# Optimization experiments

Measured on AMD Instinct MI355X. Metric: run time of the kernel, lower is better.

## Reference

```python
import jax, jax.numpy as jnp
import numpy as np

EPS_NORM = 1e-8   # torch cosine_similarity norm eps
EPS_DEN = 1e-10
CLAMP_MAX = 1e10


def _cos_matrix(a, b):
    # rows of a vs rows of b: [Na, Nb] cosine similarity via normalized matmul
    an = a / jnp.clip(jnp.linalg.norm(a, axis=-1, keepdims=True), EPS_NORM)
    bn = b / jnp.clip(jnp.linalg.norm(b, axis=-1, keepdims=True), EPS_NORM)
    return an @ bn.T


def setup_inputs() -> dict:
    key = jax.random.key(0)
    k1, k2, k3, k4, k5 = jax.random.split(key, 5)
    N, D, M, C = 4096, 256, 2, 100
    return {
        "label_encodings": jax.random.normal(k1, (N, D), dtype=jnp.float32),
        "fusion_z": jax.random.normal(k2, (M, N, D), dtype=jnp.float32),
        "sample_embeddings": jax.random.normal(k3, (N, D), dtype=jnp.float32),
        "label_embeddings": jax.random.normal(k4, (N, D), dtype=jnp.float32),
        "labels": jax.random.randint(k5, (N,), 0, C, dtype=jnp.int64),
        "temperature": jnp.ones((), dtype=jnp.float32),
        "xi": jnp.ones((), dtype=jnp.float32),
    }


def reference(label_encodings, fusion_z, sample_embeddings, label_embeddings,
              labels, temperature, xi):
    # ---- class_prompt_contrastive_Learning ----
    sim = _cos_matrix(label_encodings, label_encodings)            # [N, N]
    e = jnp.minimum(jnp.exp(sim / temperature), CLAMP_MAX)
    mask = (labels[:, None] == labels[None, :])
    num = jnp.sum(e * mask, axis=1)
    den = jnp.clip(jnp.sum(e, axis=1), EPS_DEN)
    loss_class = jnp.mean(-jnp.log(num / den))

    # ---- supervised_cross_view_contrastive ----
    M, N, D = fusion_z.shape
    fz = fusion_z.reshape(M * N, D)
    lab_exp = jnp.tile(labels, M)                                  # labels.repeat(M)
    mask2 = (lab_exp[:, None] == lab_exp[None, :])
    sim2 = _cos_matrix(fz, fz)                                     # [MN, MN]
    e2 = jnp.exp(sim2 / temperature)
    num2 = jnp.sum(e2 * mask2, axis=1)
    den2 = jnp.clip(jnp.sum(e2, axis=1), EPS_DEN)
    loss_cross = jnp.mean(-jnp.log(num2 / den2))

    # ---- boundary_aware_independent_hashing ----
    cs = _cos_matrix(sample_embeddings, label_embeddings)          # [N, N]
    Dm = (1.0 - cs) * 0.5
    y = (labels[:, None] == labels[None, :]).astype(cs.dtype)
    loss_mat = y * Dm ** 2 + (1.0 - y) * jnp.maximum(xi - Dm, 0.0) ** 2
    loss_hash = jnp.mean(loss_mat)

    return jnp.stack([loss_class, loss_cross, loss_hash])
```

## Files before the change

### kernel.cpp

```cpp
#include <hip/hip_runtime.h>
#include <hip/hip_bf16.h>
#include <stdint.h>


typedef __attribute__((ext_vector_type(8))) short bf16x8;
typedef __attribute__((ext_vector_type(4))) float f32x4;

__device__ inline void gload_lds16(const void* g, void* l) {
  __builtin_amdgcn_global_load_lds(
      (__attribute__((address_space(1))) void*)g,
      (__attribute__((address_space(3))) void*)l, 16, 0, 0);
}

__device__ inline void barrier_raw() {
  asm volatile("" ::: "memory");
  __builtin_amdgcn_s_barrier();
  asm volatile("" ::: "memory");
}

__device__ inline unsigned short f2bf(float x) {
  unsigned int u = __builtin_bit_cast(unsigned int, x);
  u = (u + 0x7fffu + ((u >> 16) & 1u)) >> 16;
  return (unsigned short)u;
}

__global__ __launch_bounds__(256) void norm_kernel(
    const float* __restrict__ LE, const float* __restrict__ FZ,
    const float* __restrict__ SE, const float* __restrict__ LM,
    unsigned short* __restrict__ An, unsigned short* __restrict__ Fn,
    unsigned short* __restrict__ Sn, unsigned short* __restrict__ Ln,
    float* __restrict__ hacc, float* __restrict__ out) {
  const int tid = threadIdx.x;
  if (blockIdx.x == 0) {
    if (tid == 0) out[0] = 0.f;
    if (tid == 1) out[1] = 0.f;
    if (tid == 2) hacc[0] = 0.f;
  }

  const int wid = tid >> 6, lane = tid & 63;
  const int row = blockIdx.x * 4 + wid;

  const float* src;
  unsigned short* dst;
  int r;
  if (row < 4096)       { src = LE; dst = An; r = row; }
  else if (row < 12288) { src = FZ; dst = Fn; r = row - 4096; }
  else if (row < 16384) { src = SE; dst = Sn; r = row - 12288; }
  else                  { src = LM; dst = Ln; r = row - 16384; }

  const float4 v = *(const float4*)(src + (size_t)r * 256 + lane * 4);
  float ss = v.x * v.x + v.y * v.y + v.z * v.z + v.w * v.w;
#pragma unroll
  for (int m = 1; m < 64; m <<= 1) ss += __shfl_xor(ss, m);
  const float scale = 1.0f / fmaxf(sqrtf(ss), 1e-8f);

  ushort4 o;
  o.x = f2bf(v.x * scale);
  o.y = f2bf(v.y * scale);
  o.z = f2bf(v.z * scale);
  o.w = f2bf(v.w * scale);
  *(ushort4*)(dst + (size_t)r * 256 + lane * 4) = o;
}

__device__ inline void tri_decode(int t, int nb, int& rb, int& cb) {
  int r = 0;
  while (t >= nb - r) { t -= nb - r; ++r; }
  rb = r;
  cb = r + t;
}

__global__ __launch_bounds__(256, 2) void fused_sim(
    const unsigned short* __restrict__ An, const unsigned short* __restrict__ Fn,
    const unsigned short* __restrict__ Sn, const unsigned short* __restrict__ Ln,
    const int* __restrict__ labels,
    const float* __restrict__ tp, const float* __restrict__ xip,
    float2* __restrict__ Pc,
    float2* __restrict__ Px,
    float* __restrict__ hacc) {
  __shared__ __align__(16) char Ab[2][16384];
  __shared__ __align__(16) char Bb[2][16384];
  __shared__ int lrS[128], lcS[128];

  const int hw = blockIdx.x;
  const int bid = (hw & 7) * 454 + (hw >> 3);

  int mode, rb, cb;
  const unsigned short *X, *Y;
  if (bid < 528) {
    mode = 0; tri_decode(bid, 32, rb, cb); X = An; Y = An;
  } else if (bid < 2608) {
    mode = 1; tri_decode(bid - 528, 64, rb, cb); X = Fn; Y = Fn;
  } else {
    mode = 2; const int t = bid - 2608; rb = t >> 5; cb = t & 31;
    X = Sn; Y = Ln;
  }

  const int tid = threadIdx.x;
  const int lane = tid & 63, wid = tid >> 6;
  const int wr = wid >> 1, wc = wid & 1;
  const int g = lane >> 4, c = lane & 15;

  int mylab = labels[(tid < 128 ? rb * 128 + tid : cb * 128 + tid - 128) & 4095];

  f32x4 acc[4][4];
  const f32x4 zero = {0.f, 0.f, 0.f, 0.f};
#pragma unroll
  for (int m = 0; m < 4; ++m)
#pragma unroll
    for (int n = 0; n < 4; ++n) acc[m][n] = zero;

  const int srow = tid >> 3;
  const int sgl = (tid & 7) ^ (srow & 7);
  const char* xs = (const char*)X + ((size_t)rb * 128 + srow) * 512 + sgl * 16;
  const char* ys = (const char*)Y + ((size_t)cb * 128 + srow) * 512 + sgl * 16;

#define STAGE(KK, BUF)                                                    \
  do {                                                                    \
    const char* xa = xs + (KK) * 128;                                     \
    const char* ya = ys + (KK) * 128;                                     \
    char* da = (char*)(&Ab[(BUF)][0]) + wid * 1024;                       \
    char* db = (char*)(&Bb[(BUF)][0]) + wid * 1024;                       \
    gload_lds16(xa, da);                                                  \
    gload_lds16(xa + 16384, da + 4096);                                   \
    gload_lds16(xa + 32768, da + 8192);                                   \
    gload_lds16(xa + 49152, da + 12288);                                  \
    gload_lds16(ya, db);                                                  \
    gload_lds16(ya + 16384, db + 4096);                                   \
    gload_lds16(ya + 32768, db + 8192);                                   \
    gload_lds16(ya + 49152, db + 12288);                                  \
  } while (0)

  STAGE(0, 0);
  STAGE(1, 1);
  asm volatile("" : "+v"(mylab));

  const int pxs = c & 7;
  const int aoff = (wr * 64 + c) * 128;
  const int boff = (wc * 64 + c) * 128;

#pragma unroll
  for (int kk = 0; kk < 4; ++kk) {
    if (kk < 3) asm volatile("s_waitcnt vmcnt(8)" ::: "memory");
    else        asm volatile("s_waitcnt vmcnt(0)" ::: "memory");
    barrier_raw();
    if (kk == 0) {
      if (tid < 128) lrS[tid] = mylab;
      else           lcS[tid - 128] = mylab;
    }
    const char* ab = (const char*)(&Ab[kk & 1][0]) + aoff;
    const char* bb = (const char*)(&Bb[kk & 1][0]) + boff;
#pragma unroll
    for (int ks = 0; ks < 2; ++ks) {
      const int px = ((ks * 4 + g) ^ pxs) * 16;
      bf16x8 af[4], bg[4];
#pragma unroll
      for (int m = 0; m < 4; ++m) af[m] = *(const bf16x8*)(ab + m * 2048 + px);
#pragma unroll
      for (int n = 0; n < 4; ++n) bg[n] = *(const bf16x8*)(bb + n * 2048 + px);
      __builtin_amdgcn_s_setprio(1);
#pragma unroll
      for (int m = 0; m < 4; ++m)
#pragma unroll
        for (int n = 0; n < 4; ++n)
          acc[m][n] = __builtin_amdgcn_mfma_f32_16x16x32_bf16(
              af[m], bg[n], acc[m][n], 0, 0, 0);
      __builtin_amdgcn_s_setprio(0);
    }
    barrier_raw();
    if (kk < 2) STAGE(kk + 2, kk & 1);
  }
#undef STAGE

  float* sc = (float*)(&Ab[0][0]);
  if (mode < 2) {
    const float invt = 1.0f / tp[0];
    const bool docol = (rb != cb);
    float2* Pp = (mode == 0) ? Pc : Px;
    const int NR = (mode == 0) ? 4096 : 8192;
    int collab[4];
#pragma unroll
    for (int n = 0; n < 4; ++n) collab[n] = lcS[wc * 64 + n * 16 + c];

    float* rowN = sc, *rowD = sc + 256, *colN = sc + 512, *colD = sc + 768;
    float cn[4] = {0.f, 0.f, 0.f, 0.f}, cd[4] = {0.f, 0.f, 0.f, 0.f};
    float rn[16], rd[16];
#pragma unroll
    for (int m = 0; m < 4; ++m) {
#pragma unroll
      for (int reg = 0; reg < 4; ++reg) {
        const int rlab = lrS[wr * 64 + m * 16 + g * 4 + reg];
        float pn = 0.f, pd = 0.f;
#pragma unroll
        for (int n = 0; n < 4; ++n) {
          float e = __expf(acc[m][n][reg] * invt);
          if (mode == 0) e = fminf(e, 1e10f);
          pd += e;
          const float en = (rlab == collab[n]) ? e : 0.f;
          pn += en;
          cd[n] += e;
          cn[n] += en;
        }
#pragma unroll
        for (int msk = 1; msk < 16; msk <<= 1) {
          pn += __shfl_xor(pn, msk);
          pd += __shfl_xor(pd, msk);
        }
        rn[m * 4 + reg] = pn;
        rd[m * 4 + reg] = pd;
      }
    }
    if (c == 0) {
#pragma unroll
      for (int m = 0; m < 4; ++m)
#pragma unroll
        for (int reg = 0; reg < 4; ++reg) {
          const int rloc = wr * 64 + m * 16 + g * 4 + reg;
          rowN[wc * 128 + rloc] = rn[m * 4 + reg];
          rowD[wc * 128 + rloc] = rd[m * 4 + reg];
        }
    }
#pragma unroll
    for (int n = 0; n < 4; ++n) {
      float a = cn[n], b = cd[n];
      a += __shfl_xor(a, 16); b += __shfl_xor(b, 16);
      a += __shfl_xor(a, 32); b += __shfl_xor(b, 32);
      if (g == 0) {
        colN[wr * 128 + wc * 64 + n * 16 + c] = a;
        colD[wr * 128 + wc * 64 + n * 16 + c] = b;
      }
    }
    __syncthreads();
    if (tid < 128) {
      Pp[(size_t)cb * NR + rb * 128 + tid] =
          make_float2(rowN[tid] + rowN[128 + tid], rowD[tid] + rowD[128 + tid]);
    } else if (docol) {
      const int t2 = tid - 128;
      Pp[(size_t)rb * NR + cb * 128 + t2] =
          make_float2(colN[t2] + colN[128 + t2], colD[t2] + colD[128 + t2]);
    }
  } else {
    const float xi = xip[0];
    int collab[4];
#pragma unroll
    for (int n = 0; n < 4; ++n) collab[n] = lcS[wc * 64 + n * 16 + c];
    float part = 0.f;
#pragma unroll
    for (int m = 0; m < 4; ++m)
#pragma unroll
      for (int reg = 0; reg < 4; ++reg) {
        const int rlab = lrS[wr * 64 + m * 16 + g * 4 + reg];
#pragma unroll
        for (int n = 0; n < 4; ++n) {
          const float cs = acc[m][n][reg];
          const float Dm = (1.0f - cs) * 0.5f;
          const float u = fmaxf(xi - Dm, 0.0f);
          part += (rlab == collab[n]) ? Dm * Dm : u * u;
        }
      }
#pragma unroll
    for (int msk = 1; msk < 64; msk <<= 1) part += __shfl_xor(part, msk);
    if (lane == 0) sc[wid] = part;
    __syncthreads();
    if (tid == 0) atomicAdd(hacc, sc[0] + sc[1] + sc[2] + sc[3]);
  }
}

__global__ __launch_bounds__(256) void finalize_kernel(
    const float2* __restrict__ Pc, const float2* __restrict__ Px,
    const float* __restrict__ hacc, float* __restrict__ out) {
  const int b = blockIdx.x, tid = threadIdx.x;
  const float2* P;
  int nslots, NR, row, oi;
  if (b < 16) { P = Pc; nslots = 32; NR = 4096; row = b * 256 + tid; oi = 0; }
  else { P = Px; nslots = 64; NR = 8192; row = (b - 16) * 256 + tid; oi = 1; }
  float n = 0.f, d = 0.f;
  for (int s = 0; s < nslots; ++s) {
    const float2 v = P[(size_t)s * NR + row];
    n += v.x;
    d += v.y;
  }
  float val = -logf(n / fmaxf(d, 1e-10f));
#pragma unroll
  for (int m = 1; m < 64; m <<= 1) val += __shfl_xor(val, m);
  __shared__ float r[4];
  if ((tid & 63) == 0) r[tid >> 6] = val;
  __syncthreads();
  if (tid == 0) atomicAdd(&out[oi], (r[0] + r[1] + r[2] + r[3]) / (float)NR);
  if (b == 0 && tid == 0) out[2] = hacc[0] * (1.0f / 16777216.0f);
}

extern "C" void kernel_launch(void* const* d_in, const int* in_sizes, int n_in,
                              void* d_out, int out_size, void* d_ws,
                              size_t ws_size, hipStream_t stream) {
  const float* LE = (const float*)d_in[0];
  const float* FZ = (const float*)d_in[1];
  const float* SE = (const float*)d_in[2];
  const float* LM = (const float*)d_in[3];
  const int* labels = (const int*)d_in[4];
  const float* tp = (const float*)d_in[5];
  const float* xip = (const float*)d_in[6];
  float* out = (float*)d_out;

  char* ws = (char*)d_ws;
  unsigned short* An = (unsigned short*)(ws);
  unsigned short* Fn = (unsigned short*)(ws + 2097152);
  unsigned short* Sn = (unsigned short*)(ws + 6291456);
  unsigned short* Ln = (unsigned short*)(ws + 8388608);
  float2* Pc = (float2*)(ws + 10485760);
  float2* Px = (float2*)(ws + 11534336);
  float* hacc = (float*)(ws + 15728640);

  norm_kernel<<<dim3(5120), dim3(256), 0, stream>>>(LE, FZ, SE, LM, An, Fn,
                                                    Sn, Ln, hacc, out);
  fused_sim<<<dim3(3632), dim3(256), 0, stream>>>(An, Fn, Sn, Ln, labels, tp,
                                                  xip, Pc, Px, hacc);
  finalize_kernel<<<dim3(48), dim3(256), 0, stream>>>(Pc, Px, hacc, out);
}
```

Baseline: 166.9 us.

## Enlarge similarity tiles to 256x256 with 512-thread blocks and interleaved prefetch

Moves the fused similarity kernel from 128x128 tiles with 256 threads to 256x256 tiles with 512 threads (8 waves, each computing a 128x64 sub-tile). The next K-slice is now prefetched inside the MFMA phases instead of after a trailing barrier, and labels are loaded straight into LDS. The aim is to halve global/L2 traffic per output, cut the number of blocks and triangular partial slots (which also shrinks the finalize reduction), and reduce barrier count. In exchange it uses 128KB+ of LDS per block, so only one block fits per CU, and it needs more accumulator registers. The 920-block grid gives less wave-level load balancing across CUs.

```diff
diff --git a/kernel.cpp b/kernel.cpp
--- a/kernel.cpp
+++ b/kernel.cpp
@@ -10,12 +10,6 @@
   __builtin_amdgcn_global_load_lds(
       (__attribute__((address_space(1))) void*)g,
       (__attribute__((address_space(3))) void*)l, 16, 0, 0);
-}
-
-__device__ inline void barrier_raw() {
-  asm volatile("" ::: "memory");
-  __builtin_amdgcn_s_barrier();
-  asm volatile("" ::: "memory");
 }
 
 __device__ inline unsigned short f2bf(float x) {
@@ -69,7 +63,7 @@
   cb = r + t;
 }
 
-__global__ __launch_bounds__(256, 2) void fused_sim(
+__global__ __launch_bounds__(512) void fused_sim(
     const unsigned short* __restrict__ An, const unsigned short* __restrict__ Fn,
     const unsigned short* __restrict__ Sn, const unsigned short* __restrict__ Ln,
     const int* __restrict__ labels,
@@ -77,103 +71,119 @@
     float2* __restrict__ Pc,
     float2* __restrict__ Px,
     float* __restrict__ hacc) {
-  __shared__ __align__(16) char Ab[2][16384];
-  __shared__ __align__(16) char Bb[2][16384];
-  __shared__ int lrS[128], lcS[128];
+  __shared__ __align__(16) char AB[131072];
+  __shared__ __align__(16) int labS[512];
+  __shared__ float sN[1024], sD[1024];
+  __shared__ float cN[512], cD[512];
+
+  const int tid = threadIdx.x;
+  const int lane = tid & 63, wid = tid >> 6;
+  const int wr = wid >> 2, wc = wid & 3;
+  const int g = lane >> 4, c = lane & 15;
 
   const int hw = blockIdx.x;
-  const int bid = (hw & 7) * 454 + (hw >> 3);
+  const int bid = (hw & 7) * 115 + (hw >> 3);
 
   int mode, rb, cb;
   const unsigned short *X, *Y;
-  if (bid < 528) {
-    mode = 0; tri_decode(bid, 32, rb, cb); X = An; Y = An;
-  } else if (bid < 2608) {
-    mode = 1; tri_decode(bid - 528, 64, rb, cb); X = Fn; Y = Fn;
+  if (bid < 136) {
+    mode = 0; tri_decode(bid, 16, rb, cb); X = An; Y = An;
+  } else if (bid < 664) {
+    mode = 1; tri_decode(bid - 136, 32, rb, cb); X = Fn; Y = Fn;
   } else {
-    mode = 2; const int t = bid - 2608; rb = t >> 5; cb = t & 31;
+    mode = 2; const int t = bid - 664; rb = t >> 4; cb = t & 15;
     X = Sn; Y = Ln;
   }
 
-  const int tid = threadIdx.x;
-  const int lane = tid & 63, wid = tid >> 6;
-  const int wr = wid >> 1, wc = wid & 1;
-  const int g = lane >> 4, c = lane & 15;
-
-  int mylab = labels[(tid < 128 ? rb * 128 + tid : cb * 128 + tid - 128) & 4095];
-
-  f32x4 acc[4][4];
-  const f32x4 zero = {0.f, 0.f, 0.f, 0.f};
-#pragma unroll
-  for (int m = 0; m < 4; ++m)
-#pragma unroll
-    for (int n = 0; n < 4; ++n) acc[m][n] = zero;
+  const float invt = 1.0f / tp[0];
+  const float xi = xip[0];
 
   const int srow = tid >> 3;
   const int sgl = (tid & 7) ^ (srow & 7);
-  const char* xs = (const char*)X + ((size_t)rb * 128 + srow) * 512 + sgl * 16;
-  const char* ys = (const char*)Y + ((size_t)cb * 128 + srow) * 512 + sgl * 16;
-
-#define STAGE(KK, BUF)                                                    \
+  const char* xsA =
+      (const char*)X + ((size_t)rb * 256 + srow) * 512 + sgl * 16;
+  const char* ysB =
+      (const char*)Y + ((size_t)cb * 256 + srow) * 512 + sgl * 16;
+
+  const int px0 = c & 7;
+  const char* aBase = AB + (wr * 128 + c) * 128;
+  const char* bBase = AB + 32768 + (wc * 64 + c) * 128;
+
+#define STG_A(KT)                                                         \
   do {                                                                    \
-    const char* xa = xs + (KK) * 128;                                     \
-    const char* ya = ys + (KK) * 128;                                     \
-    char* da = (char*)(&Ab[(BUF)][0]) + wid * 1024;                       \
-    char* db = (char*)(&Bb[(BUF)][0]) + wid * 1024;                       \
-    gload_lds16(xa, da);                                                  \
-    gload_lds16(xa + 16384, da + 4096);                                   \
-    gload_lds16(xa + 32768, da + 8192);                                   \
-    gload_lds16(xa + 49152, da + 12288);                                  \
-    gload_lds16(ya, db);                                                  \
-    gload_lds16(ya + 16384, db + 4096);                                   \
-    gload_lds16(ya + 32768, db + 8192);                                   \
-    gload_lds16(ya + 49152, db + 12288);                                  \
+    const char* s_ = xsA + (KT) * 128;                                    \
+    char* d_ = AB + (((KT) & 1) * 65536) + wid * 1024;                    \
+    gload_lds16(s_, d_);                                                  \
+    gload_lds16(s_ + 32768, d_ + 8192);                                   \
+    gload_lds16(s_ + 65536, d_ + 16384);                                  \
+    gload_lds16(s_ + 98304, d_ + 24576);                                  \
   } while (0)
-
-  STAGE(0, 0);
-  STAGE(1, 1);
-  asm volatile("" : "+v"(mylab));
-
-  const int pxs = c & 7;
-  const int aoff = (wr * 64 + c) * 128;
-  const int boff = (wc * 64 + c) * 128;
-
-#pragma unroll
-  for (int kk = 0; kk < 4; ++kk) {
-    if (kk < 3) asm volatile("s_waitcnt vmcnt(8)" ::: "memory");
-    else        asm volatile("s_waitcnt vmcnt(0)" ::: "memory");
-    barrier_raw();
-    if (kk == 0) {
-      if (tid < 128) lrS[tid] = mylab;
-      else           lcS[tid - 128] = mylab;
-    }
-    const char* ab = (const char*)(&Ab[kk & 1][0]) + aoff;
-    const char* bb = (const char*)(&Bb[kk & 1][0]) + boff;
-#pragma unroll
-    for (int ks = 0; ks < 2; ++ks) {
-      const int px = ((ks * 4 + g) ^ pxs) * 16;
-      bf16x8 af[4], bg[4];
-#pragma unroll
-      for (int m = 0; m < 4; ++m) af[m] = *(const bf16x8*)(ab + m * 2048 + px);
-#pragma unroll
-      for (int n = 0; n < 4; ++n) bg[n] = *(const bf16x8*)(bb + n * 2048 + px);
+#define STG_B(KT)                                                         \
+  do {                                                                    \
+    const char* s_ = ysB + (KT) * 128;                                    \
+    char* d_ = AB + (((KT) & 1) * 65536) + 32768 + wid * 1024;            \
+    gload_lds16(s_, d_);                                                  \
+    gload_lds16(s_ + 32768, d_ + 8192);                                   \
+    gload_lds16(s_ + 65536, d_ + 16384);                                  \
+    gload_lds16(s_ + 98304, d_ + 24576);                                  \
+  } while (0)
+
+  {
+    const char* lr = (const char*)labels + (rb & 15) * 1024 + lane * 16;
+    const char* lc = (const char*)labels + (cb & 15) * 1024 + lane * 16;
+    gload_lds16(lr, (char*)labS);
+    gload_lds16(lc, (char*)labS + 1024);
+  }
+  STG_A(0);
+  STG_B(0);
+
+  f32x4 acc[8][4];
+  const f32x4 zero = {0.f, 0.f, 0.f, 0.f};
+#pragma unroll
+  for (int m = 0; m < 8; ++m)
+#pragma unroll
+    for (int n = 0; n < 4; ++n) acc[m][n] = zero;
+  bf16x8 af[4], bg[4];
+
+#pragma unroll
+  for (int kt = 0; kt < 4; ++kt) {
+    asm volatile("s_waitcnt vmcnt(0)" ::: "memory");
+    __builtin_amdgcn_s_barrier();
+    asm volatile("" ::: "memory");
+    const int bo = (kt & 1) * 65536;
+#pragma unroll
+    for (int ph = 0; ph < 4; ++ph) {
+      const int ks = ph >> 1, mh = ph & 1;
+      const int px = ((ks * 4 + g) ^ px0) * 16;
+#pragma unroll
+      for (int m = 0; m < 4; ++m)
+        af[m] = *(const bf16x8*)(aBase + bo + mh * 8192 + m * 2048 + px);
+      if (mh == 0) {
+#pragma unroll
+        for (int n = 0; n < 4; ++n)
+          bg[n] = *(const bf16x8*)(bBase + bo + n * 2048 + px);
+      }
+      if (kt < 3) {
+        if (ph == 0) STG_A(kt + 1);
+        else if (ph == 1) STG_B(kt + 1);
+      }
+      asm volatile("s_waitcnt lgkmcnt(0)" ::: "memory");
       __builtin_amdgcn_s_setprio(1);
 #pragma unroll
       for (int m = 0; m < 4; ++m)
 #pragma unroll
         for (int n = 0; n < 4; ++n)
-          acc[m][n] = __builtin_amdgcn_mfma_f32_16x16x32_bf16(
-              af[m], bg[n], acc[m][n], 0, 0, 0);
+          acc[mh * 4 + m][n] = __builtin_amdgcn_mfma_f32_16x16x32_bf16(
+              af[m], bg[n], acc[mh * 4 + m][n], 0, 0, 0);
       __builtin_amdgcn_s_setprio(0);
     }
-    barrier_raw();
-    if (kk < 2) STAGE(kk + 2, kk & 1);
-  }
-#undef STAGE
-
-  float* sc = (float*)(&Ab[0][0]);
+  }
+#undef STG_A
+#undef STG_B
+
+  const int* lrS = labS;
+  const int* lcS = labS + 256;
   if (mode < 2) {
-    const float invt = 1.0f / tp[0];
     const bool docol = (rb != cb);
     float2* Pp = (mode == 0) ? Pc : Px;
     const int NR = (mode == 0) ? 4096 : 8192;
@@ -181,14 +191,13 @@
 #pragma unroll
     for (int n = 0; n < 4; ++n) collab[n] = lcS[wc * 64 + n * 16 + c];
 
-    float* rowN = sc, *rowD = sc + 256, *colN = sc + 512, *colD = sc + 768;
     float cn[4] = {0.f, 0.f, 0.f, 0.f}, cd[4] = {0.f, 0.f, 0.f, 0.f};
-    float rn[16], rd[16];
-#pragma unroll
-    for (int m = 0; m < 4; ++m) {
+#pragma unroll
+    for (int m = 0; m < 8; ++m) {
 #pragma unroll
       for (int reg = 0; reg < 4; ++reg) {
-        const int rlab = lrS[wr * 64 + m * 16 + g * 4 + reg];
+        const int rloc = wr * 128 + m * 16 + g * 4 + reg;
+        const int rlab = lrS[rloc];
         float pn = 0.f, pd = 0.f;
 #pragma unroll
         for (int n = 0; n < 4; ++n) {
@@ -205,19 +214,11 @@
           pn += __shfl_xor(pn, msk);
           pd += __shfl_xor(pd, msk);
         }
-        rn[m * 4 + reg] = pn;
-        rd[m * 4 + reg] = pd;
-      }
-    }
-    if (c == 0) {
-#pragma unroll
-      for (int m = 0; m < 4; ++m)
-#pragma unroll
-        for (int reg = 0; reg < 4; ++reg) {
-          const int rloc = wr * 64 + m * 16 + g * 4 + reg;
-          rowN[wc * 128 + rloc] = rn[m * 4 + reg];
-          rowD[wc * 128 + rloc] = rd[m * 4 + reg];
+        if (c == 0) {
+          sN[wc * 256 + rloc] = pn;
+          sD[wc * 256 + rloc] = pd;
         }
+      }
     }
 #pragma unroll
     for (int n = 0; n < 4; ++n) {
@@ -225,30 +226,32 @@
       a += __shfl_xor(a, 16); b += __shfl_xor(b, 16);
       a += __shfl_xor(a, 32); b += __shfl_xor(b, 32);
       if (g == 0) {
-        colN[wr * 128 + wc * 64 + n * 16 + c] = a;
-        colD[wr * 128 + wc * 64 + n * 16 + c] = b;
-      }
-    }
-    __syncthreads();
-    if (tid < 128) {
-      Pp[(size_t)cb * NR + rb * 128 + tid] =
-          make_float2(rowN[tid] + rowN[128 + tid], rowD[tid] + rowD[128 + tid]);
+        cN[wr * 256 + wc * 64 + n * 16 + c] = a;
+        cD[wr * 256 + wc * 64 + n * 16 + c] = b;
+      }
+    }
+    asm volatile("s_waitcnt lgkmcnt(0)" ::: "memory");
+    __builtin_amdgcn_s_barrier();
+    asm volatile("" ::: "memory");
+    if (tid < 256) {
+      Pp[(size_t)cb * NR + rb * 256 + tid] = make_float2(
+          sN[tid] + sN[256 + tid] + sN[512 + tid] + sN[768 + tid],
+          sD[tid] + sD[256 + tid] + sD[512 + tid] + sD[768 + tid]);
     } else if (docol) {
-      const int t2 = tid - 128;
-      Pp[(size_t)rb * NR + cb * 128 + t2] =
-          make_float2(colN[t2] + colN[128 + t2], colD[t2] + colD[128 + t2]);
+      const int t2 = tid - 256;
+      Pp[(size_t)rb * NR + cb * 256 + t2] =
+          make_float2(cN[t2] + cN[256 + t2], cD[t2] + cD[256 + t2]);
     }
   } else {
-    const float xi = xip[0];
     int collab[4];
 #pragma unroll
     for (int n = 0; n < 4; ++n) collab[n] = lcS[wc * 64 + n * 16 + c];
     float part = 0.f;
 #pragma unroll
-    for (int m = 0; m < 4; ++m)
+    for (int m = 0; m < 8; ++m)
 #pragma unroll
       for (int reg = 0; reg < 4; ++reg) {
-        const int rlab = lrS[wr * 64 + m * 16 + g * 4 + reg];
+        const int rlab = lrS[wr * 128 + m * 16 + g * 4 + reg];
 #pragma unroll
         for (int n = 0; n < 4; ++n) {
           const float cs = acc[m][n][reg];
@@ -259,9 +262,16 @@
       }
 #pragma unroll
     for (int msk = 1; msk < 64; msk <<= 1) part += __shfl_xor(part, msk);
-    if (lane == 0) sc[wid] = part;
-    __syncthreads();
-    if (tid == 0) atomicAdd(hacc, sc[0] + sc[1] + sc[2] + sc[3]);
+    if (lane == 0) sN[wid] = part;
+    asm volatile("s_waitcnt lgkmcnt(0)" ::: "memory");
+    __builtin_amdgcn_s_barrier();
+    asm volatile("" ::: "memory");
+    if (tid == 0) {
+      float s = 0.f;
+#pragma unroll
+      for (int w = 0; w < 8; ++w) s += sN[w];
+      atomicAdd(hacc, s);
+    }
   }
 }
 
@@ -271,8 +281,8 @@
   const int b = blockIdx.x, tid = threadIdx.x;
   const float2* P;
   int nslots, NR, row, oi;
-  if (b < 16) { P = Pc; nslots = 32; NR = 4096; row = b * 256 + tid; oi = 0; }
-  else { P = Px; nslots = 64; NR = 8192; row = (b - 16) * 256 + tid; oi = 1; }
+  if (b < 16) { P = Pc; nslots = 16; NR = 4096; row = b * 256 + tid; oi = 0; }
+  else { P = Px; nslots = 32; NR = 8192; row = (b - 16) * 256 + tid; oi = 1; }
   float n = 0.f, d = 0.f;
   for (int s = 0; s < nslots; ++s) {
     const float2 v = P[(size_t)s * NR + row];
@@ -312,7 +322,7 @@
 
   norm_kernel<<<dim3(5120), dim3(256), 0, stream>>>(LE, FZ, SE, LM, An, Fn,
                                                     Sn, Ln, hacc, out);
-  fused_sim<<<dim3(3632), dim3(256), 0, stream>>>(An, Fn, Sn, Ln, labels, tp,
-                                                  xip, Pc, Px, hacc);
+  fused_sim<<<dim3(920), dim3(512), 0, stream>>>(An, Fn, Sn, Ln, labels, tp,
+                                                 xip, Pc, Px, hacc);
   finalize_kernel<<<dim3(48), dim3(256), 0, stream>>>(Pc, Px, hacc, out);
 }
```

After: 167.7 us. About the same (+0.5%).
